# Kernel tuning notes

Hardware: AMD Instinct MI355X
Metric: run time of the kernel (lower is better)

The kernel has to match this reference:

```python
import jax, jax.numpy as jnp
import numpy as np
from jax.scipy.special import logsumexp

B, S, D, T = 32, 512, 768, 9


def setup_inputs() -> dict:
    key = jax.random.key(0)
    ks = jax.random.split(key, 12)
    s = 0.05
    return {
        "x": jax.random.normal(ks[0], (B, S, D), jnp.float32),
        "tags": jax.random.randint(ks[1], (B, S), 0, T, jnp.int32),
        "mask": jnp.ones((B, S), jnp.bool_),
        "w_ih_f": jax.random.normal(ks[2], (4 * D, D), jnp.float32) * s,
        "w_hh_f": jax.random.normal(ks[3], (4 * D, D), jnp.float32) * s,
        "b_f": jnp.zeros((4 * D,), jnp.float32),
        "w_ih_b": jax.random.normal(ks[4], (4 * D, D), jnp.float32) * s,
        "w_hh_b": jax.random.normal(ks[5], (4 * D, D), jnp.float32) * s,
        "b_b": jnp.zeros((4 * D,), jnp.float32),
        "w_cls": jax.random.normal(ks[6], (T, 2 * D), jnp.float32) * s,
        "b_cls": jnp.zeros((T,), jnp.float32),
        "transitions": jax.random.normal(ks[7], (T, T), jnp.float32) * 0.1,
        "start_trans": jax.random.normal(ks[8], (T,), jnp.float32) * 0.1,
        "end_trans": jax.random.normal(ks[9], (T,), jnp.float32) * 0.1,
    }


def _lstm_dir(x, w_ih, w_hh, b):
    # x: [B,S,D] -> hidden states [B,S,H]; PyTorch gate order i,f,g,o.
    Bb, Ss, _ = x.shape
    H = w_hh.shape[1]
    xg = jnp.einsum('bsd,gd->bsg', x, w_ih) + b  # precompute input projections [B,S,4H]

    def step(carry, xg_t):
        h, c = carry
        g = xg_t + h @ w_hh.T
        i, f, gg, o = jnp.split(g, 4, axis=-1)
        c = jax.nn.sigmoid(f) * c + jax.nn.sigmoid(i) * jnp.tanh(gg)
        h = jax.nn.sigmoid(o) * jnp.tanh(c)
        return (h, c), h

    init = (jnp.zeros((Bb, H), x.dtype), jnp.zeros((Bb, H), x.dtype))
    _, hs = jax.lax.scan(step, init, jnp.swapaxes(xg, 0, 1))  # time-major scan
    return jnp.swapaxes(hs, 0, 1)


def _crf_loss(emissions, tags, mask, transitions, start_trans, end_trans):
    # emissions [B,S,T]; negative token-mean log-likelihood (pytorch-crf).
    mf = mask.astype(emissions.dtype)
    # ---- numerator: score of the gold path (fully vectorized) ----
    em = jnp.take_along_axis(emissions, tags[..., None], axis=-1)[..., 0]  # [B,S]
    tr = transitions[tags[:, :-1], tags[:, 1:]]                            # [B,S-1]
    num = start_trans[tags[:, 0]] + em[:, 0]
    num = num + jnp.sum((tr + em[:, 1:]) * mf[:, 1:], axis=1)
    last_idx = jnp.sum(mask.astype(jnp.int32), axis=1) - 1
    last_tags = jnp.take_along_axis(tags, last_idx[:, None], axis=1)[:, 0]
    num = num + end_trans[last_tags]
    # ---- denominator: forward algorithm via scan over time ----
    score0 = start_trans + emissions[:, 0]  # [B,T]

    def step(score, inp):
        em_t, m_t = inp  # [B,T], [B]
        nxt = logsumexp(score[:, :, None] + transitions[None] + em_t[:, None, :], axis=1)
        return jnp.where(m_t[:, None], nxt, score), None

    em_tm = jnp.swapaxes(emissions[:, 1:], 0, 1)  # [S-1,B,T]
    m_tm = jnp.swapaxes(mask[:, 1:], 0, 1)        # [S-1,B]
    score, _ = jax.lax.scan(step, score0, (em_tm, m_tm))
    den = logsumexp(score + end_trans, axis=1)
    llh = num - den
    return -(jnp.sum(llh) / jnp.sum(mf))  # reduction='token_mean', negated


def reference(x, tags, mask, w_ih_f, w_hh_f, b_f, w_ih_b, w_hh_b, b_b,
              w_cls, b_cls, transitions, start_trans, end_trans):
    h_f = _lstm_dir(x, w_ih_f, w_hh_f, b_f)
    h_b = _lstm_dir(x[:, ::-1], w_ih_b, w_hh_b, b_b)[:, ::-1]
    h = jnp.concatenate([h_f, h_b], axis=-1)          # [B,S,2D]
    emissions = h @ w_cls.T + b_cls                   # [B,S,T]
    return _crf_loss(emissions, tags, mask, transitions, start_trans, end_trans)
```

## Files before the change

### kernel.cpp

```cpp
#include <hip/hip_runtime.h>
#include <stdint.h>

#define BB 32
#define SS 512
#define DD 768
#define GG 3072
#define NTAG 9
#define BSR (BB*SS)
#define EMS 12
#define FLS 4

typedef __attribute__((ext_vector_type(8))) short bf16x8;
typedef __attribute__((ext_vector_type(4))) float f32x4;

__device__ __forceinline__ float b2f(unsigned short s) {
    union { unsigned u; float f; } v; v.u = ((unsigned)s) << 16; return v.f;
}
__device__ __forceinline__ unsigned short f2b(float f) {
    union { float f; unsigned u; } v; v.f = f;
    unsigned r = v.u + 0x7FFFu + ((v.u >> 16) & 1u);
    return (unsigned short)(r >> 16);
}
__device__ __forceinline__ int pack2(float a, float b) {
    return (int)f2b(a) | ((int)f2b(b) << 16);
}
__device__ __forceinline__ float sigm_(float x) { return 1.f / (1.f + __expf(-x)); }
__device__ __forceinline__ float tanh_(float x) {
    float e = __expf(2.f * x);
    return 1.f - 2.f / (e + 1.f);
}

__global__ void k_diag(float* out, float v) { out[0] = v; }

__global__ void k_permw(const float* __restrict__ src, unsigned short* __restrict__ dst) {
    int gp = blockIdx.x;
    int g = (gp & 3) * DD + (gp >> 2);
    const float* s = src + (size_t)g * DD;
    unsigned short* d = dst + (size_t)gp * DD;
    for (int j = threadIdx.x; j < DD; j += blockDim.x) d[j] = f2b(s[j]);
}
__global__ void k_permb(const float* __restrict__ src, float* __restrict__ dst) {
    int gp = blockIdx.x * blockDim.x + threadIdx.x;
    if (gp < GG) dst[gp] = src[(gp & 3) * DD + (gp >> 2)];
}

#define BM 128
#define BN 128
#define BK 32
__global__ __launch_bounds__(256, 2) void k_gemm_xg(
    const float* __restrict__ X,
    const unsigned short* __restrict__ Wp,
    const float* __restrict__ bias,
    unsigned short* __restrict__ Xg,
    int rev)
{
    __shared__ unsigned short As[BM * BK];
    __shared__ unsigned short Bs[BN * BK];
    int tid = threadIdx.x;
    int lane = tid & 63, w = tid >> 6;
    int wm = w >> 1, wn = w & 1;
    int rowBase = blockIdx.x * BM;
    int colBase = blockIdx.y * BN;

    f32x4 acc[4][4];
#pragma unroll
    for (int mf = 0; mf < 4; ++mf)
#pragma unroll
        for (int nf = 0; nf < 4; ++nf) { acc[mf][nf][0]=0.f; acc[mf][nf][1]=0.f; acc[mf][nf][2]=0.f; acc[mf][nf][3]=0.f; }

    for (int kt = 0; kt < DD / BK; ++kt) {
#pragma unroll
        for (int c = 0; c < 2; ++c) {
            int id = tid * 2 + c;
            int r = id >> 2, ko = id & 3;
            int rowg = rowBase + r;
            int srow;
            if (rev) { int b = rowg >> 9, t = rowg & 511; srow = b * SS + (SS - 1 - t); }
            else srow = rowg;
            const float* src = X + (size_t)srow * DD + kt * BK + ko * 8;
            float4 v0 = *(const float4*)(src);
            float4 v1 = *(const float4*)(src + 4);
            int blk = ko ^ ((r >> 1) & 3);
            *(int4*)(&As[r * BK + blk * 8]) =
                make_int4(pack2(v0.x, v0.y), pack2(v0.z, v0.w), pack2(v1.x, v1.y), pack2(v1.z, v1.w));
        }
#pragma unroll
        for (int c = 0; c < 2; ++c) {
            int id = tid * 2 + c;
            int r = id >> 2, ko = id & 3;
            int4 v = *(const int4*)(Wp + (size_t)(colBase + r) * DD + kt * BK + ko * 8);
            int blk = ko ^ ((r >> 1) & 3);
            *(int4*)(&Bs[r * BK + blk * 8]) = v;
        }
        __syncthreads();
        bf16x8 af[4], bfr[4];
        int ko = lane >> 4;
#pragma unroll
        for (int mf = 0; mf < 4; ++mf) {
            int r = wm * 64 + mf * 16 + (lane & 15);
            af[mf] = *(const bf16x8*)(&As[r * BK + (ko ^ ((r >> 1) & 3)) * 8]);
        }
#pragma unroll
        for (int nf = 0; nf < 4; ++nf) {
            int r = wn * 64 + nf * 16 + (lane & 15);
            bfr[nf] = *(const bf16x8*)(&Bs[r * BK + (ko ^ ((r >> 1) & 3)) * 8]);
        }
#pragma unroll
        for (int mf = 0; mf < 4; ++mf)
#pragma unroll
            for (int nf = 0; nf < 4; ++nf)
                acc[mf][nf] = __builtin_amdgcn_mfma_f32_16x16x32_bf16(af[mf], bfr[nf], acc[mf][nf], 0, 0, 0);
        __syncthreads();
    }
#pragma unroll
    for (int mf = 0; mf < 4; ++mf)
#pragma unroll
        for (int nf = 0; nf < 4; ++nf) {
            int colg = colBase + wn * 64 + nf * 16 + (lane & 15);
            float bv = bias[colg];
#pragma unroll
            for (int i = 0; i < 4; ++i) {
                int rowg = rowBase + wm * 64 + mf * 16 + (lane >> 4) * 4 + i;
                Xg[(size_t)rowg * GG + colg] = f2b(acc[mf][nf][i] + bv);
            }
        }
}

#define NWG 64
#define GR 48
__global__ __launch_bounds__(384, 1) void k_lstm(
    const unsigned short* __restrict__ xg_f, const unsigned short* __restrict__ xg_b,
    const unsigned short* __restrict__ whh_f, const unsigned short* __restrict__ whh_b,
    unsigned short* __restrict__ hs_f, unsigned short* __restrict__ hs_b,
    unsigned int* __restrict__ flags)
{
    int bid = blockIdx.x;
    int dir = bid >> 6;
    int wg = bid & 63;
    const unsigned short* xg = dir ? xg_b : xg_f;
    const unsigned short* whh = dir ? whh_b : whh_f;
    unsigned short* hs = dir ? hs_b : hs_f;
    unsigned int* flgD = flags + (size_t)dir * SS * 64 * FLS;

    int tid = threadIdx.x;
    int lane = tid & 63, w = tid >> 6;
    int mt = w >> 1, nt = w & 1;
    int g0 = wg * GR;
    int ko = lane >> 4;

    int wrow = g0 + mt * 16 + (lane & 15);
    bf16x8 wf[24];
#pragma unroll
    for (int kt = 0; kt < 24; ++kt)
        wf[kt] = *(const bf16x8*)(whh + (size_t)wrow * DD + kt * 32 + ko * 8);

    int bcol = nt * 16 + (lane & 15);
    int g4 = wg * 12 + mt * 4;
    int gp4 = g0 + mt * 16 + ko * 4;
    const unsigned short* xgrow = xg + (size_t)bcol * SS * GG + gp4;
    unsigned short* hrow = hs + (size_t)bcol * SS * DD;
    float c = 0.f;

    short4 xv = *(const short4*)xgrow;
    for (int t = 0; t < SS; ++t) {
        f32x4 acc;
        acc[0] = b2f((unsigned short)xv.x);
        acc[1] = b2f((unsigned short)xv.y);
        acc[2] = b2f((unsigned short)xv.z);
        acc[3] = b2f((unsigned short)xv.w);
        if (t > 0) {
            const unsigned short* hb = hrow + (size_t)(t - 1) * DD + ko * 8;
#pragma unroll
            for (int kt = 0; kt < 24; ++kt) {
                bf16x8 hv = *(const bf16x8*)(hb + kt * 32);
                acc = __builtin_amdgcn_mfma_f32_16x16x32_bf16(wf[kt], hv, acc, 0, 0, 0);
            }
        }
        float si = sigm_(acc[0]);
        float sf = sigm_(acc[1]);
        float tg = tanh_(acc[2]);
        float so = sigm_(acc[3]);
        c = sf * c + si * tg;
        float h = so * tanh_(c);

        unsigned short hb16 = f2b(h);
        unsigned short pb16 = (unsigned short)__shfl_xor((int)hb16, 16, 64);
        unsigned hp = (unsigned)hb16 | ((unsigned)pb16 << 16);
        unsigned hp2 = (unsigned)__shfl_xor((int)hp, 32, 64);
        if (ko == 0) {
            unsigned long long v8 = ((unsigned long long)hp2 << 32) | (unsigned long long)hp;
            __hip_atomic_store((unsigned long long*)(hrow + (size_t)t * DD + g4), v8,
                               __ATOMIC_RELAXED, __HIP_MEMORY_SCOPE_AGENT);
        }

        if (t == SS - 1) break;

        asm volatile("s_waitcnt vmcnt(0)" ::: "memory");
        __syncthreads();
        if (tid == 0)
            __hip_atomic_store(flgD + (size_t)t * 64 * FLS + wg * FLS, 1u,
                               __ATOMIC_RELAXED, __HIP_MEMORY_SCOPE_AGENT);

        xv = *(const short4*)(xgrow + (size_t)(t + 1) * GG);

        if (w == 0) {
            const unsigned int* fp = flgD + (size_t)t * 64 * FLS + lane * FLS;
            while (__hip_atomic_load(fp, __ATOMIC_RELAXED, __HIP_MEMORY_SCOPE_AGENT) == 0)
                __builtin_amdgcn_s_sleep(1);
        }
        __syncthreads();
        asm volatile("" ::: "memory");
    }
}

__global__ void k_emis(const unsigned short* __restrict__ hs_f, const unsigned short* __restrict__ hs_b,
                       const float* __restrict__ wcls, const float* __restrict__ bcls,
                       float* __restrict__ em)
{
    int row = blockIdx.x * 4 + (threadIdx.x >> 6);
    int lane = threadIdx.x & 63;
    int b = row >> 9, t = row & 511;
    const unsigned long long* hfq = (const unsigned long long*)(hs_f + (size_t)row * DD);
    const unsigned long long* hbq = (const unsigned long long*)(hs_b + ((size_t)(b * SS + (SS - 1 - t))) * DD);
    float p[NTAG];
#pragma unroll
    for (int tau = 0; tau < NTAG; ++tau) p[tau] = 0.f;
#pragma unroll
    for (int it = 0; it < 3; ++it) {
        int j4 = lane + it * 64;
        unsigned long long af = hfq[j4];
        unsigned long long ab = hbq[j4];
#pragma unroll
        for (int e = 0; e < 4; ++e) {
            int j = j4 * 4 + e;
            float hv  = b2f((unsigned short)(af >> (16 * e)));
            float hv2 = b2f((unsigned short)(ab >> (16 * e)));
#pragma unroll
            for (int tau = 0; tau < NTAG; ++tau) {
                p[tau] += hv * wcls[tau * 2 * DD + j];
                p[tau] += hv2 * wcls[tau * 2 * DD + DD + j];
            }
        }
    }
#pragma unroll
    for (int tau = 0; tau < NTAG; ++tau) {
        float v = p[tau];
        for (int m = 32; m; m >>= 1) v += __shfl_xor(v, m, 64);
        if (lane == 0) em[(size_t)row * EMS + tau] = v + bcls[tau];
    }
}

__global__ void k_crf(const float* __restrict__ em, const int* __restrict__ tags,
                      const float* __restrict__ trans, const float* __restrict__ start_t,
                      const float* __restrict__ end_t, float* __restrict__ llh)
{
    int b = blockIdx.x;
    int lane = threadIdx.x;
    const int* tg = tags + b * SS;
    const float* emb = em + (size_t)b * SS * EMS;

    float np = 0.f;
    for (int it = 0; it < 8; ++it) {
        int t = 1 + lane + it * 64;
        if (t < SS) {
            int t0 = tg[t - 1], t1 = tg[t];
            np += trans[t0 * NTAG + t1] + emb[t * EMS + t1];
        }
    }
    for (int m = 32; m; m >>= 1) np += __shfl_xor(np, m, 64);

    float score, ec;
    float tc[NTAG];
    if (lane < NTAG) {
        score = start_t[lane] + emb[lane];
        ec = end_t[lane];
#pragma unroll
        for (int i = 0; i < NTAG; ++i) tc[i] = trans[i * NTAG + lane];
    } else {
        score = -1e30f; ec = 0.f;
#pragma unroll
        for (int i = 0; i < NTAG; ++i) tc[i] = 0.f;
    }
    int eidx = (lane < NTAG) ? lane : 0;
    for (int t = 1; t < SS; ++t) {
        float vv[NTAG];
        float mx = -1e30f;
#pragma unroll
        for (int i = 0; i < NTAG; ++i) {
            float si = __shfl(score, i, 64);
            vv[i] = si + tc[i];
            mx = fmaxf(mx, vv[i]);
        }
        float sum = 0.f;
#pragma unroll
        for (int i = 0; i < NTAG; ++i) sum += __expf(vv[i] - mx);
        float ns = mx + __logf(sum) + emb[t * EMS + eidx];
        score = (lane < NTAG) ? ns : -1e30f;
    }
    float sv = (lane < NTAG) ? score + ec : -1e30f;
    float mx = sv;
    for (int m = 32; m; m >>= 1) mx = fmaxf(mx, __shfl_xor(mx, m, 64));
    float se = (lane < NTAG) ? __expf(sv - mx) : 0.f;
    for (int m = 32; m; m >>= 1) se += __shfl_xor(se, m, 64);
    float den = mx + __logf(se);
    if (lane == 0) {
        float num = np + start_t[tg[0]] + emb[tg[0]] + end_t[tg[SS - 1]];
        llh[b] = num - den;
    }
}

__global__ void k_loss(const float* __restrict__ llh, float* __restrict__ out) {
    int lane = threadIdx.x;
    float v = (lane < BB) ? llh[lane] : 0.f;
    for (int m = 32; m; m >>= 1) v += __shfl_xor(v, m, 64);
    if (lane == 0) out[0] = -v / (float)(BB * SS);
}

extern "C" void kernel_launch(void* const* d_in, const int* in_sizes, int n_in,
                              void* d_out, int out_size, void* d_ws, size_t ws_size,
                              hipStream_t stream) {
    (void)in_sizes; (void)n_in; (void)out_size;
    const float* x      = (const float*)d_in[0];
    const int* tags     = (const int*)d_in[1];
    const float* wihF   = (const float*)d_in[3];
    const float* whhF   = (const float*)d_in[4];
    const float* bF     = (const float*)d_in[5];
    const float* wihB   = (const float*)d_in[6];
    const float* whhB   = (const float*)d_in[7];
    const float* bBi    = (const float*)d_in[8];
    const float* wcls   = (const float*)d_in[9];
    const float* bcls   = (const float*)d_in[10];
    const float* trans  = (const float*)d_in[11];
    const float* startT = (const float*)d_in[12];
    const float* endT   = (const float*)d_in[13];
    float* out = (float*)d_out;

    const size_t szW  = (size_t)GG * DD * 2;
    const size_t szB  = GG * 4;
    const size_t szXg = (size_t)BSR * GG * 2;
    const size_t szHs = (size_t)BB * SS * DD * 2;
    const size_t szEm = (size_t)BSR * EMS * 4;
    const size_t szFl = (size_t)2 * SS * 64 * FLS * 4;
    const size_t NEED = 3*szW + 2*szB + 2*szXg + 2*szHs + szEm + szFl + 8192;

    if (ws_size < NEED) {
        k_diag<<<1, 1, 0, stream>>>(out, (float)(ws_size >> 20));
        return;
    }

    char* wp = (char*)d_ws;
    auto alloc = [&](size_t bytes) { char* p = wp; wp += (bytes + 255) & ~(size_t)255; return p; };
    unsigned short* whhFp = (unsigned short*)alloc(szW);
    unsigned short* whhBp = (unsigned short*)alloc(szW);
    unsigned short* wihP  = (unsigned short*)alloc(szW);
    float* bFp = (float*)alloc(szB);
    float* bBp = (float*)alloc(szB);
    unsigned short* hsF = (unsigned short*)alloc(szHs);
    unsigned short* hsB = (unsigned short*)alloc(szHs);
    float* em  = (float*)alloc(szEm);
    float* llh = (float*)alloc(256);
    unsigned int* flags = (unsigned int*)alloc(szFl);
    unsigned short* xgF = (unsigned short*)alloc(szXg);
    unsigned short* xgB = (unsigned short*)alloc(szXg);

    k_permw<<<GG, 256, 0, stream>>>(whhF, whhFp);
    k_permw<<<GG, 256, 0, stream>>>(whhB, whhBp);
    k_permb<<<GG / 256, 256, 0, stream>>>(bF, bFp);
    k_permb<<<GG / 256, 256, 0, stream>>>(bBi, bBp);
    hipMemsetAsync(flags, 0, szFl, stream);

    dim3 gg(BSR / BM, GG / BN);
    k_permw<<<GG, 256, 0, stream>>>(wihF, wihP);
    k_gemm_xg<<<gg, 256, 0, stream>>>(x, wihP, bFp, xgF, 0);
    k_permw<<<GG, 256, 0, stream>>>(wihB, wihP);
    k_gemm_xg<<<gg, 256, 0, stream>>>(x, wihP, bBp, xgB, 1);

    k_lstm<<<2 * NWG, 384, 0, stream>>>(xgF, xgB, whhFp, whhBp, hsF, hsB, flags);

    k_emis<<<BSR / 4, 256, 0, stream>>>(hsF, hsB, wcls, bcls, em);
    k_crf<<<BB, 64, 0, stream>>>(em, tags, trans, startT, endT, llh);
    k_loss<<<1, 64, 0, stream>>>(llh, out);
}
```

Measured before the change: 4.016 ms.

## Place each LSTM direction's workgroups on a single XCC via dynamic claiming

The recurrent LSTM kernel now launches many more workgroups than it needs. Each workgroup reads its hardware XCC id and claims a (direction, slot) pair through atomic counters, so that forward-direction groups land on XCC 0 and backward-direction groups on XCC 1, with a fallback for late arrivals; surplus groups exit immediately. When all 64 groups of a direction end up on the same XCC, hidden-state writes switch from agent-scope atomic stores to plain stores. The aim is to keep the per-step cross-workgroup exchange inside one XCC's L2 and cut coherence traffic, at the cost of extra launch and claim overhead and a dependence on how the hardware schedules workgroups.

```diff
diff --git a/kernel.cpp b/kernel.cpp
--- a/kernel.cpp
+++ b/kernel.cpp
@@ -9,6 +9,10 @@
 #define BSR (BB*SS)
 #define EMS 12
 #define FLS 4
+#define NWG 64
+#define GR 48
+#define CLAIMG 512
+#define XCC_GETREG ((31 << 11) | 20)
 
 typedef __attribute__((ext_vector_type(8))) short bf16x8;
 typedef __attribute__((ext_vector_type(4))) float f32x4;
@@ -126,24 +130,55 @@
         }
 }
 
-#define NWG 64
-#define GR 48
 __global__ __launch_bounds__(384, 1) void k_lstm(
     const unsigned short* __restrict__ xg_f, const unsigned short* __restrict__ xg_b,
     const unsigned short* __restrict__ whh_f, const unsigned short* __restrict__ whh_b,
     unsigned short* __restrict__ hs_f, unsigned short* __restrict__ hs_b,
-    unsigned int* __restrict__ flags)
+    unsigned int* __restrict__ flags,
+    unsigned int* __restrict__ claim)
 {
-    int bid = blockIdx.x;
-    int dir = bid >> 6;
-    int wg = bid & 63;
+    __shared__ int sDir, sWg, sXcc, sFast;
+    int tid = threadIdx.x;
+    int lane = tid & 63, w = tid >> 6;
+
+    if (tid == 0) {
+        unsigned xcc = __builtin_amdgcn_s_getreg(XCC_GETREG);
+        unsigned arrived = __hip_atomic_fetch_add(&claim[0], 1u, __ATOMIC_RELAXED, __HIP_MEMORY_SCOPE_AGENT);
+        int dir = -1, wg = -1;
+        int late = (arrived >= (unsigned)(CLAIMG - 140));
+        if (xcc == 0u || late) {
+            unsigned s = __hip_atomic_fetch_add(&claim[8], 1u, __ATOMIC_RELAXED, __HIP_MEMORY_SCOPE_AGENT);
+            if (s < NWG) { dir = 0; wg = (int)s; }
+        }
+        if (dir < 0 && (xcc == 1u || late)) {
+            unsigned s = __hip_atomic_fetch_add(&claim[16], 1u, __ATOMIC_RELAXED, __HIP_MEMORY_SCOPE_AGENT);
+            if (s < NWG) { dir = 1; wg = (int)s; }
+        }
+        if (dir >= 0)
+            __hip_atomic_store(&claim[32 + dir * NWG + wg], xcc + 1u,
+                               __ATOMIC_RELAXED, __HIP_MEMORY_SCOPE_AGENT);
+        sDir = dir; sWg = wg; sXcc = (int)xcc;
+    }
+    __syncthreads();
+    int dir = sDir, wg = sWg;
+    if (dir < 0) return;
+
+    if (w == 0) {
+        const unsigned int* sl = &claim[32 + dir * NWG + lane];
+        unsigned v;
+        while ((v = __hip_atomic_load(sl, __ATOMIC_RELAXED, __HIP_MEMORY_SCOPE_AGENT)) == 0u)
+            __builtin_amdgcn_s_sleep(2);
+        unsigned long long ok = __ballot(v == (unsigned)(sXcc + 1));
+        if (lane == 0) sFast = (ok == ~0ULL) ? 1 : 0;
+    }
+    __syncthreads();
+    int fast = sFast;
+
     const unsigned short* xg = dir ? xg_b : xg_f;
     const unsigned short* whh = dir ? whh_b : whh_f;
     unsigned short* hs = dir ? hs_b : hs_f;
     unsigned int* flgD = flags + (size_t)dir * SS * 64 * FLS;
 
-    int tid = threadIdx.x;
-    int lane = tid & 63, w = tid >> 6;
     int mt = w >> 1, nt = w & 1;
     int g0 = wg * GR;
     int ko = lane >> 4;
@@ -189,8 +224,9 @@
         unsigned hp2 = (unsigned)__shfl_xor((int)hp, 32, 64);
         if (ko == 0) {
             unsigned long long v8 = ((unsigned long long)hp2 << 32) | (unsigned long long)hp;
-            __hip_atomic_store((unsigned long long*)(hrow + (size_t)t * DD + g4), v8,
-                               __ATOMIC_RELAXED, __HIP_MEMORY_SCOPE_AGENT);
+            unsigned long long* dst = (unsigned long long*)(hrow + (size_t)t * DD + g4);
+            if (fast) *dst = v8;
+            else __hip_atomic_store(dst, v8, __ATOMIC_RELAXED, __HIP_MEMORY_SCOPE_AGENT);
         }
 
         if (t == SS - 1) break;
@@ -341,7 +377,8 @@
     const size_t szHs = (size_t)BB * SS * DD * 2;
     const size_t szEm = (size_t)BSR * EMS * 4;
     const size_t szFl = (size_t)2 * SS * 64 * FLS * 4;
-    const size_t NEED = 3*szW + 2*szB + 2*szXg + 2*szHs + szEm + szFl + 8192;
+    const size_t szCl = 4096;
+    const size_t NEED = 3*szW + 2*szB + 2*szXg + 2*szHs + szEm + szFl + szCl + 8192;
 
     if (ws_size < NEED) {
         k_diag<<<1, 1, 0, stream>>>(out, (float)(ws_size >> 20));
@@ -360,6 +397,7 @@
     float* em  = (float*)alloc(szEm);
     float* llh = (float*)alloc(256);
     unsigned int* flags = (unsigned int*)alloc(szFl);
+    unsigned int* claim = (unsigned int*)alloc(szCl);
     unsigned short* xgF = (unsigned short*)alloc(szXg);
     unsigned short* xgB = (unsigned short*)alloc(szXg);
 
@@ -368,6 +406,7 @@
     k_permb<<<GG / 256, 256, 0, stream>>>(bF, bFp);
     k_permb<<<GG / 256, 256, 0, stream>>>(bBi, bBp);
     hipMemsetAsync(flags, 0, szFl, stream);
+    hipMemsetAsync(claim, 0, szCl, stream);
 
     dim3 gg(BSR / BM, GG / BN);
     k_permw<<<GG, 256, 0, stream>>>(wihF, wihP);
@@ -375,7 +414,7 @@
     k_permw<<<GG, 256, 0, stream>>>(wihB, wihP);
     k_gemm_xg<<<gg, 256, 0, stream>>>(x, wihP, bBp, xgB, 1);
 
-    k_lstm<<<2 * NWG, 384, 0, stream>>>(xgF, xgB, whhFp, whhBp, hsF, hsB, flags);
+    k_lstm<<<CLAIMG, 384, 0, stream>>>(xgF, xgB, whhFp, whhBp, hsF, hsB, flags, claim);
 
     k_emis<<<BSR / 4, 256, 0, stream>>>(hsF, hsB, wcls, bcls, em);
     k_crf<<<BB, 64, 0, stream>>>(em, tags, trans, startT, endT, llh);
```

After: 6.290 ms. 56.6% more time.
